# Performance work log

Hardware: AMD Instinct MI355X
Metric: run time of the kernel (lower is better)

The kernel has to match this reference:

```python
import jax, jax.numpy as jnp
import numpy as np


def setup_inputs() -> dict:
    key = jax.random.key(0)
    k1, k2 = jax.random.split(key)
    B, N, M, D = 8, 8192, 8192, 3
    input1 = jax.random.normal(k1, (B, N, D), dtype=jnp.float32)
    input2 = jax.random.normal(k2, (B, M, D), dtype=jnp.float32)
    return {"input1": input1, "input2": input2}


def reference(input1, input2):
    # input1: [B, N, 3], input2: [B, M, 3]
    # Squared pairwise distances via ||x||^2 + ||y||^2 - 2<x,y>
    sq1 = jnp.sum(input1 * input1, axis=-1)          # [B, N]
    sq2 = jnp.sum(input2 * input2, axis=-1)          # [B, M]
    inner = jnp.einsum('bnd,bmd->bnm', input1, input2)  # [B, N, M]
    d = sq1[:, :, None] + sq2[:, None, :] - 2.0 * inner  # [B, N, M]
    d = jnp.maximum(d, 0.0)  # numerical guard
    dist1 = jnp.min(d, axis=2)  # [B, N] NN in input2 for each point of input1
    dist2 = jnp.min(d, axis=1)  # [B, M] NN in input1 for each point of input2
    loss = jnp.mean(dist1) + jnp.mean(dist2)
    return loss
```

## Files before the change

kernel.cpp:

```cpp
#include <hip/hip_runtime.h>


typedef _Float16 half8 __attribute__((ext_vector_type(8)));
typedef float    f16x  __attribute__((ext_vector_type(16)));

constexpr int B       = 8;
constexpr int NPTS    = 8192;
constexpr int TOTAL   = B * NPTS;
constexpr int NSTRIP  = 128;
constexpr int NSTRIPS = NPTS / NSTRIP;
constexpr int MH      = 4;
constexpr int MHALF   = NPTS / MH;
constexpr int CHUNK   = 512;
constexpr int NWAVE   = 4;

__device__ __forceinline__ float colmin16(const f16x& a)
{
    float m0 = fminf(fminf(a[0],  a[1]),  a[2]);
    float m1 = fminf(fminf(a[3],  a[4]),  a[5]);
    float m2 = fminf(fminf(a[6],  a[7]),  a[8]);
    float m3 = fminf(fminf(a[9],  a[10]), a[11]);
    float m4 = fminf(fminf(a[12], a[13]), a[14]);
    return fminf(fminf(fminf(m0, m1), m2), fminf(fminf(m3, m4), a[15]));
}

__global__ __launch_bounds__(256, 5) void chamfer_mfma(
    const float* __restrict__ in1, const float* __restrict__ in2,
    float* __restrict__ d1p, float* __restrict__ d2p, float* __restrict__ out)
{
    const int b     = blockIdx.z;
    const int strip = blockIdx.x;
    const int mh    = blockIdx.y;
    const int wave  = threadIdx.x >> 6;
    const int lane  = threadIdx.x & 63;
    const int col   = lane & 31;
    const int half  = lane >> 5;

    if ((blockIdx.x | blockIdx.y | blockIdx.z) == 0 && threadIdx.x == 0)
        *out = 0.0f;

    __shared__ _Float16 ldsB[CHUNK * 16];
    __shared__ float    d2w[NWAVE][CHUNK];

    const int nbase = strip * NSTRIP + wave * 32;
    half8 afrag;
    {
        const float* a = in1 + ((size_t)b * NPTS + nbase + col) * 3;
        float x = a[0], y = a[1], z = a[2];
        float sq = fmaf(x, x, fmaf(y, y, z * z));
        _Float16 xh = (_Float16)x, yh = (_Float16)y, zh = (_Float16)z;
        _Float16 xl = (_Float16)(x - (float)xh);
        _Float16 yl = (_Float16)(y - (float)yh);
        _Float16 zl = (_Float16)(z - (float)zh);
        _Float16 sh = (_Float16)sq, sl = (_Float16)(sq - (float)sh);
        half8 lo = {xh, yh, zh, xl, yl, zl, xh, yh};
        half8 hi = {zh, sh, sl, (_Float16)1.f, (_Float16)1.f,
                    (_Float16)0.f, (_Float16)0.f, (_Float16)0.f};
        afrag = half ? hi : lo;
    }

    f16x MN1, zero;
#pragma unroll
    for (int r = 0; r < 16; ++r) { MN1[r] = 1e30f; zero[r] = 0.0f; }

    const float* Craw = in2 + ((size_t)b * NPTS + mh * MHALF) * 3;
    float* d2 = d2p + ((size_t)b * NSTRIPS + strip) * NPTS + mh * MHALF;

    for (int c = 0; c < MHALF / CHUNK; ++c) {
        __syncthreads();
#pragma unroll
        for (int s = 0; s < 2; ++s) {
            const int i = threadIdx.x + s * 256;
            const float* cp = Craw + (size_t)(c * CHUNK + i) * 3;
            float cx = cp[0], cy = cp[1], cz = cp[2];
            float x = -2.f * cx, y = -2.f * cy, z = -2.f * cz;
            float sq = fmaf(cx, cx, fmaf(cy, cy, cz * cz));
            _Float16 xh = (_Float16)x, yh = (_Float16)y, zh = (_Float16)z;
            _Float16 xl = (_Float16)(x - (float)xh);
            _Float16 yl = (_Float16)(y - (float)yh);
            _Float16 zl = (_Float16)(z - (float)zh);
            _Float16 sh = (_Float16)sq, sl = (_Float16)(sq - (float)sh);
            half8 lo = {xh, yh, zh, xh, yh, zh, xl, yl};
            half8 hi = {zl, (_Float16)1.f, (_Float16)1.f, sh, sl,
                        (_Float16)0.f, (_Float16)0.f, (_Float16)0.f};
            *(half8*)&ldsB[i * 16]     = lo;
            *(half8*)&ldsB[i * 16 + 8] = hi;
        }
        if (c > 0) {
#pragma unroll
            for (int s = 0; s < 2; ++s) {
                const int i = threadIdx.x + s * 256;
                float v = fminf(fminf(d2w[0][i], d2w[1][i]),
                                fminf(d2w[2][i], d2w[3][i]));
                d2[(c - 1) * CHUNK + i] = fmaxf(v, 0.0f);
            }
        }
        __syncthreads();

#pragma unroll 2
        for (int t = 0; t < CHUNK / 32; t += 2) {
            half8 bfA = *(const half8*)&ldsB[((t    ) * 32 + col) * 16 + half * 8];
            half8 bfB = *(const half8*)&ldsB[((t + 1) * 32 + col) * 16 + half * 8];
            f16x accA = __builtin_amdgcn_mfma_f32_32x32x16_f16(afrag, bfA, zero, 0, 0, 0);
            f16x accB = __builtin_amdgcn_mfma_f32_32x32x16_f16(afrag, bfB, zero, 0, 0, 0);

#pragma unroll
            for (int r = 0; r < 16; ++r)
                MN1[r] = fminf(fminf(accA[r], accB[r]), MN1[r]);

            float vA = colmin16(accA);
            float vB = colmin16(accB);
            vA = fminf(vA, __shfl_xor(vA, 32, 64));
            vB = fminf(vB, __shfl_xor(vB, 32, 64));
            d2w[wave][t * 32 + lane] = half ? vB : vA;
        }
    }
    __syncthreads();
#pragma unroll
    for (int s = 0; s < 2; ++s) {
        const int i = threadIdx.x + s * 256;
        float v = fminf(fminf(d2w[0][i], d2w[1][i]),
                        fminf(d2w[2][i], d2w[3][i]));
        d2[(MHALF / CHUNK - 1) * CHUNK + i] = fmaxf(v, 0.0f);
    }

#pragma unroll
    for (int m = 1; m <= 16; m <<= 1)
#pragma unroll
        for (int r = 0; r < 16; ++r)
            MN1[r] = fminf(MN1[r], __shfl_xor(MN1[r], m, 64));
    if (col == 0) {
        float* d1 = d1p + ((size_t)b * MH + mh) * NPTS + nbase;
#pragma unroll
        for (int r = 0; r < 16; ++r)
            d1[(r & 3) + 8 * (r >> 2) + 4 * half] = MN1[r];
    }
}

__global__ __launch_bounds__(64) void reduce_kernel(
    const float* __restrict__ d1p, const float* __restrict__ d2p,
    float* __restrict__ out)
{
    int g  = blockIdx.x * 64 + threadIdx.x;
    int b  = g >> 11;
    int mq = g & 2047;

    const float4* p2 = (const float4*)(d2p + (size_t)b * NSTRIPS * NPTS) + mq;
    float4 v2 = p2[0];
#pragma unroll 8
    for (int s = 1; s < NSTRIPS; ++s) {
        float4 t = p2[(size_t)s * (NPTS / 4)];
        v2.x = fminf(v2.x, t.x); v2.y = fminf(v2.y, t.y);
        v2.z = fminf(v2.z, t.z); v2.w = fminf(v2.w, t.w);
    }
    const float4* p1 = (const float4*)(d1p + (size_t)b * MH * NPTS) + mq;
    float4 a = p1[0];
#pragma unroll
    for (int s = 1; s < MH; ++s) {
        float4 t = p1[(size_t)s * (NPTS / 4)];
        a.x = fminf(a.x, t.x); a.y = fminf(a.y, t.y);
        a.z = fminf(a.z, t.z); a.w = fminf(a.w, t.w);
    }
    float v = fmaxf(a.x, 0.0f) + fmaxf(a.y, 0.0f)
            + fmaxf(a.z, 0.0f) + fmaxf(a.w, 0.0f)
            + v2.x + v2.y + v2.z + v2.w;

#pragma unroll
    for (int off = 32; off; off >>= 1)
        v += __shfl_down(v, off, 64);
    if (threadIdx.x == 0)
        atomicAdd(out, v * (1.0f / (float)TOTAL));
}

extern "C" void kernel_launch(void* const* d_in, const int* in_sizes, int n_in,
                              void* d_out, int out_size, void* d_ws, size_t ws_size,
                              hipStream_t stream)
{
    const float* in1 = (const float*)d_in[0];
    const float* in2 = (const float*)d_in[1];
    float* out = (float*)d_out;

    char* ws = (char*)d_ws;
    float* d1p = (float*)ws;
    float* d2p = (float*)(ws + (size_t)MH * TOTAL * 4);

    chamfer_mfma<<<dim3(NSTRIPS, MH, B), 256, 0, stream>>>(
        in1, in2, d1p, d2p, out);
    reduce_kernel<<<TOTAL / 4 / 64, 64, 0, stream>>>(d1p, d2p, out);
}
```

Baseline: 105.9 us.

## Use 512-thread blocks with 256-row strips and reorganize LDS B-fragment layout

Doubles the rows per block to 256 (8 waves) and halves the M split to 2, so each staged chunk of input2 is reused by twice as many waves and there are half as many d2 partial strips to reduce. The LDS layout for B fragments is changed so each MFMA operand load reads contiguous 16-byte-per-lane data indexed by lane, aiming to avoid bank conflicts. The trade-offs are a larger block with a lower occupancy bound, longer per-block work and an 8-way cross-wave min at each chunk boundary.

After: 97.45 us. -8.0%, faster.

```diff
diff --git a/kernel.cpp b/kernel.cpp
--- a/kernel.cpp
+++ b/kernel.cpp
@@ -7,12 +7,12 @@
 constexpr int B       = 8;
 constexpr int NPTS    = 8192;
 constexpr int TOTAL   = B * NPTS;
-constexpr int NSTRIP  = 128;
+constexpr int NSTRIP  = 256;
 constexpr int NSTRIPS = NPTS / NSTRIP;
-constexpr int MH      = 4;
+constexpr int MH      = 2;
 constexpr int MHALF   = NPTS / MH;
 constexpr int CHUNK   = 512;
-constexpr int NWAVE   = 4;
+constexpr int NWAVE   = 8;
 
 __device__ __forceinline__ float colmin16(const f16x& a)
 {
@@ -24,7 +24,7 @@
     return fminf(fminf(fminf(m0, m1), m2), fminf(fminf(m3, m4), a[15]));
 }
 
-__global__ __launch_bounds__(256, 5) void chamfer_mfma(
+__global__ __launch_bounds__(512, 4) void chamfer_mfma(
     const float* __restrict__ in1, const float* __restrict__ in2,
     float* __restrict__ d1p, float* __restrict__ d2p, float* __restrict__ out)
 {
@@ -59,18 +59,17 @@
         afrag = half ? hi : lo;
     }
 
-    f16x MN1, zero;
+    f16x MN1, zacc;
 #pragma unroll
-    for (int r = 0; r < 16; ++r) { MN1[r] = 1e30f; zero[r] = 0.0f; }
+    for (int r = 0; r < 16; ++r) { MN1[r] = 1e30f; zacc[r] = 0.0f; }
 
     const float* Craw = in2 + ((size_t)b * NPTS + mh * MHALF) * 3;
     float* d2 = d2p + ((size_t)b * NSTRIPS + strip) * NPTS + mh * MHALF;
 
     for (int c = 0; c < MHALF / CHUNK; ++c) {
         __syncthreads();
-#pragma unroll
-        for (int s = 0; s < 2; ++s) {
-            const int i = threadIdx.x + s * 256;
+        {
+            const int i = threadIdx.x;
             const float* cp = Craw + (size_t)(c * CHUNK + i) * 3;
             float cx = cp[0], cy = cp[1], cz = cp[2];
             float x = -2.f * cx, y = -2.f * cy, z = -2.f * cz;
@@ -83,26 +82,24 @@
             half8 lo = {xh, yh, zh, xh, yh, zh, xl, yl};
             half8 hi = {zl, (_Float16)1.f, (_Float16)1.f, sh, sl,
                         (_Float16)0.f, (_Float16)0.f, (_Float16)0.f};
-            *(half8*)&ldsB[i * 16]     = lo;
-            *(half8*)&ldsB[i * 16 + 8] = hi;
+            *(half8*)&ldsB[(i >> 5) * 512 + (i & 31) * 8]       = lo;
+            *(half8*)&ldsB[(i >> 5) * 512 + 256 + (i & 31) * 8] = hi;
         }
         if (c > 0) {
+            const int i = threadIdx.x;
+            float v = d2w[0][i];
 #pragma unroll
-            for (int s = 0; s < 2; ++s) {
-                const int i = threadIdx.x + s * 256;
-                float v = fminf(fminf(d2w[0][i], d2w[1][i]),
-                                fminf(d2w[2][i], d2w[3][i]));
-                d2[(c - 1) * CHUNK + i] = fmaxf(v, 0.0f);
-            }
+            for (int w = 1; w < NWAVE; ++w) v = fminf(v, d2w[w][i]);
+            d2[(c - 1) * CHUNK + i] = fmaxf(v, 0.0f);
         }
         __syncthreads();
 
 #pragma unroll 2
         for (int t = 0; t < CHUNK / 32; t += 2) {
-            half8 bfA = *(const half8*)&ldsB[((t    ) * 32 + col) * 16 + half * 8];
-            half8 bfB = *(const half8*)&ldsB[((t + 1) * 32 + col) * 16 + half * 8];
-            f16x accA = __builtin_amdgcn_mfma_f32_32x32x16_f16(afrag, bfA, zero, 0, 0, 0);
-            f16x accB = __builtin_amdgcn_mfma_f32_32x32x16_f16(afrag, bfB, zero, 0, 0, 0);
+            half8 bfA = *(const half8*)&ldsB[ t      * 512 + lane * 8];
+            half8 bfB = *(const half8*)&ldsB[(t + 1) * 512 + lane * 8];
+            f16x accA = __builtin_amdgcn_mfma_f32_32x32x16_f16(afrag, bfA, zacc, 0, 0, 0);
+            f16x accB = __builtin_amdgcn_mfma_f32_32x32x16_f16(afrag, bfB, zacc, 0, 0, 0);
 
 #pragma unroll
             for (int r = 0; r < 16; ++r)
@@ -112,15 +109,15 @@
             float vB = colmin16(accB);
             vA = fminf(vA, __shfl_xor(vA, 32, 64));
             vB = fminf(vB, __shfl_xor(vB, 32, 64));
-            d2w[wave][t * 32 + lane] = half ? vB : vA;
+            d2w[wave][(t + half) * 32 + col] = half ? vB : vA;
         }
     }
     __syncthreads();
+    {
+        const int i = threadIdx.x;
+        float v = d2w[0][i];
 #pragma unroll
-    for (int s = 0; s < 2; ++s) {
-        const int i = threadIdx.x + s * 256;
-        float v = fminf(fminf(d2w[0][i], d2w[1][i]),
-                        fminf(d2w[2][i], d2w[3][i]));
+        for (int w = 1; w < NWAVE; ++w) v = fminf(v, d2w[w][i]);
         d2[(MHALF / CHUNK - 1) * CHUNK + i] = fmaxf(v, 0.0f);
     }
 
@@ -184,7 +181,7 @@
     float* d1p = (float*)ws;
     float* d2p = (float*)(ws + (size_t)MH * TOTAL * 4);
 
-    chamfer_mfma<<<dim3(NSTRIPS, MH, B), 256, 0, stream>>>(
+    chamfer_mfma<<<dim3(NSTRIPS, MH, B), 512, 0, stream>>>(
         in1, in2, d1p, d2p, out);
     reduce_kernel<<<TOTAL / 4 / 64, 64, 0, stream>>>(d1p, d2p, out);
 }
```
